# Optimization experiments

Measured on AMD Instinct MI355X. Metric: run time of the kernel, lower is better.

Reference implementation:

```python
import jax, jax.numpy as jnp
import numpy as np

N_EMBD = 1024
N_HEAD = 16


def setup_inputs() -> dict:
    key = jax.random.key(0)
    k1, k2, k3 = jax.random.split(key, 3)
    B, T, C = 4, 2048, N_EMBD
    x = jax.random.normal(k1, (B, T, C), dtype=jnp.float32)
    # params (bias=False)
    w_attn = jax.random.normal(k2, (C, 3 * C), dtype=jnp.float32) * (C ** -0.5)
    w_proj = jax.random.normal(k3, (C, C), dtype=jnp.float32) * (C ** -0.5)
    return {"x": x, "w_attn": w_attn, "w_proj": w_proj}


def reference(x, w_attn, w_proj):
    B, T, C = x.shape
    H = N_HEAD
    hs = C // H
    qkv = x @ w_attn  # [B,T,3C]
    q, k, v = jnp.split(qkv, 3, axis=-1)
    # [B,H,T,hs]
    q = q.reshape(B, T, H, hs).transpose(0, 2, 1, 3)
    k = k.reshape(B, T, H, hs).transpose(0, 2, 1, 3)
    v = v.reshape(B, T, H, hs).transpose(0, 2, 1, 3)
    wei = jnp.einsum('bhqd,bhkd->bhqk', q, k) * (hs ** -0.5)
    causal = jnp.tril(jnp.ones((T, T), dtype=bool))
    wei = jnp.where(causal[None, None], wei, -jnp.inf)
    wei = jax.nn.softmax(wei, axis=-1)
    # dropout p=0.0 -> identity
    y = jnp.einsum('bhqk,bhkd->bhqd', wei, v)
    y = y.transpose(0, 2, 1, 3).reshape(B, T, C)
    return y @ w_proj
```

## Files before the change

### kernel.cpp

```cpp
#include <hip/hip_runtime.h>
#include <math.h>
#include <stdint.h>

#define B_BATCH 4
#define T_SEQ   2048
#define C_EMB   1024
#define NH      16
#define HS      64

typedef _Float16 half_t;
typedef __attribute__((ext_vector_type(8))) _Float16 half8;
typedef __attribute__((ext_vector_type(4))) _Float16 half4;
typedef __attribute__((ext_vector_type(2))) __fp16 pk16x2;
typedef __attribute__((ext_vector_type(4))) float f32x4;

static __device__ __forceinline__ f32x4 mfma_k16(half4 a, half4 b, f32x4 c) {
#if __has_builtin(__builtin_amdgcn_mfma_f32_16x16x16f16)
    return __builtin_amdgcn_mfma_f32_16x16x16f16(a, b, c, 0, 0, 0);
#else
    half8 a8 = {a.x, a.y, a.z, a.w, (_Float16)0, (_Float16)0, (_Float16)0, (_Float16)0};
    half8 b8 = {b.x, b.y, b.z, b.w, (_Float16)0, (_Float16)0, (_Float16)0, (_Float16)0};
    return __builtin_amdgcn_mfma_f32_16x16x32_f16(a8, b8, c, 0, 0, 0);
#endif
}

static __device__ __forceinline__ void stage16(const void* g, void* lds_base) {
#if __has_builtin(__builtin_amdgcn_global_load_lds)
    __builtin_amdgcn_global_load_lds(
        (const __attribute__((address_space(1))) void*)g,
        (__attribute__((address_space(3))) void*)lds_base, 16, 0, 0);
#else
    const int lane = threadIdx.x & 63;
    ((uint4*)lds_base)[lane] = *(const uint4*)g;
#endif
}

__global__ __launch_bounds__(256) void prep_kernel(const float* __restrict__ x,
                                                   half_t* __restrict__ xh,
                                                   const float* __restrict__ wa,
                                                   half_t* __restrict__ waT,
                                                   const float* __restrict__ wp,
                                                   half_t* __restrict__ wpT) {
    const int blk = blockIdx.x;
    const int tid = threadIdx.x;

    if (blk < 4096) {
        const int i = blk * 256 + tid;
        const float4 a = *(const float4*)(x + (size_t)i * 8);
        const float4 b = *(const float4*)(x + (size_t)i * 8 + 4);
        const pk16x2 h0 = __builtin_amdgcn_cvt_pkrtz(a.x, a.y);
        const pk16x2 h1 = __builtin_amdgcn_cvt_pkrtz(a.z, a.w);
        const pk16x2 h2 = __builtin_amdgcn_cvt_pkrtz(b.x, b.y);
        const pk16x2 h3 = __builtin_amdgcn_cvt_pkrtz(b.z, b.w);
        half8 o = {(_Float16)h0.x, (_Float16)h0.y, (_Float16)h1.x, (_Float16)h1.y,
                   (_Float16)h2.x, (_Float16)h2.y, (_Float16)h3.x, (_Float16)h3.y};
        *(half8*)(xh + (size_t)i * 8) = o;
        return;
    }

    const float* W;
    half_t* WT;
    int K, N, bb;
    if (blk < 4096 + 768) {
        bb = blk - 4096; W = wa; WT = waT; K = 1024; N = 3072;
    } else {
        bb = blk - 4864; W = wp; WT = wpT; K = 1024; N = 1024;
    }
    const int ntiles = N / 64;
    const int n0 = (bb % ntiles) * 64;
    const int k0 = (bb / ntiles) * 64;

    __shared__ float t[64][65];
    const int r = tid >> 4, c4 = (tid & 15) * 4;
#pragma unroll
    for (int p = 0; p < 4; ++p) {
        const float4 g = *(const float4*)(W + (size_t)(k0 + p * 16 + r) * N + n0 + c4);
        t[p * 16 + r][c4 + 0] = g.x;
        t[p * 16 + r][c4 + 1] = g.y;
        t[p * 16 + r][c4 + 2] = g.z;
        t[p * 16 + r][c4 + 3] = g.w;
    }
    __syncthreads();
#pragma unroll
    for (int p = 0; p < 4; ++p) {
        const int n = p * 16 + r;
        half4 s = {(_Float16)t[c4 + 0][n], (_Float16)t[c4 + 1][n],
                   (_Float16)t[c4 + 2][n], (_Float16)t[c4 + 3][n]};
        *(half4*)(WT + (size_t)(n0 + n) * K + k0 + c4) = s;
    }
}

#define BK2 64

__global__ __launch_bounds__(512, 2) void gemm256(const half_t* __restrict__ A,
                                                  const half_t* __restrict__ Bt,
                                                  half_t* __restrict__ Cout,
                                                  int M, int N, int K) {
    __shared__ __align__(16) half_t SM[65536];

    const int tid  = threadIdx.x;
    const int lane = tid & 63;
    const int wid  = tid >> 6;
    const int l16  = lane & 15;
    const int quad = lane >> 4;

    const int nwg = gridDim.x;
    const int cpx = nwg >> 3;
    const int bid = (blockIdx.x & 7) * cpx + (blockIdx.x >> 3);
    const int nbx = N >> 8;
    const int bx = bid % nbx;
    const int by = bid / nbx;
    const size_t m0 = (size_t)by << 8;
    const size_t n0 = (size_t)bx << 8;

    const int warpM = (wid >> 2) * 128;
    const int wn    = (wid & 3) * 64;
    const int NTk   = K >> 6;

    const int srow = tid >> 3;
    const int scsw = (tid & 7) ^ (srow & 7);
    const half_t* gAs = A  + (m0 + srow) * (size_t)K + scsw * 8;
    const half_t* gBs = Bt + (n0 + srow) * (size_t)K + scsw * 8;

    f32x4 acc[8][4];
#pragma unroll
    for (int i = 0; i < 8; ++i)
#pragma unroll
        for (int j = 0; j < 4; ++j) acc[i][j] = (f32x4){0.f, 0.f, 0.f, 0.f};

    auto ldA = [&](const half_t* Ab, int mt, int kk) -> half8 {
        const int r = warpM + mt * 16 + l16;
        const int c = (kk * 4 + quad) ^ (l16 & 7);
        return *(const half8*)(Ab + r * 64 + c * 8);
    };
    auto ldB = [&](const half_t* Bb, int nt, int kk) -> half8 {
        const int r = wn + nt * 16 + l16;
        const int c = (kk * 4 + quad) ^ (l16 & 7);
        return *(const half8*)(Bb + r * 64 + c * 8);
    };

#pragma unroll
    for (int s = 0; s < 4; ++s)
        stage16(gAs + (size_t)(s * 64) * K, SM + s * 4096 + wid * 512);
#pragma unroll
    for (int s = 0; s < 4; ++s)
        stage16(gBs + (size_t)(s * 64) * K, SM + 16384 + s * 4096 + wid * 512);
    if (NTk > 1) {
#pragma unroll
        for (int s = 0; s < 4; ++s)
            stage16(gBs + (size_t)(s * 64) * K + BK2, SM + 49152 + s * 4096 + wid * 512);
        asm volatile("s_waitcnt vmcnt(4)" ::: "memory");
    } else {
        asm volatile("s_waitcnt vmcnt(0)" ::: "memory");
    }
    __builtin_amdgcn_s_barrier();
    __builtin_amdgcn_sched_barrier(0);

    auto tile_body = [&](int t, half_t* Ac, half_t* Bc, half_t* An) {
        const int kA = (t + 1) * BK2;
        const int kB = (t + 2) * BK2;
        const bool doA = (t + 1) < NTk;
        const bool doB = (t + 2) < NTk;

        half8 fb[4][2];

        if (doA) {
            stage16(gAs + (size_t)(0 * 64) * K + kA, An + 0 * 4096 + wid * 512);
            stage16(gAs + (size_t)(1 * 64) * K + kA, An + 1 * 4096 + wid * 512);
        }
#pragma unroll
        for (int nt = 0; nt < 4; ++nt) {
            fb[nt][0] = ldB(Bc, nt, 0);
            fb[nt][1] = ldB(Bc, nt, 1);
        }
        {
            half8 a00 = ldA(Ac, 0, 0), a01 = ldA(Ac, 0, 1);
            half8 a10 = ldA(Ac, 1, 0), a11 = ldA(Ac, 1, 1);
            __builtin_amdgcn_s_barrier();
            __builtin_amdgcn_s_setprio(1);
#pragma unroll
            for (int nt = 0; nt < 4; ++nt) {
                acc[0][nt] = __builtin_amdgcn_mfma_f32_16x16x32_f16(a00, fb[nt][0], acc[0][nt], 0, 0, 0);
                acc[0][nt] = __builtin_amdgcn_mfma_f32_16x16x32_f16(a01, fb[nt][1], acc[0][nt], 0, 0, 0);
                acc[1][nt] = __builtin_amdgcn_mfma_f32_16x16x32_f16(a10, fb[nt][0], acc[1][nt], 0, 0, 0);
                acc[1][nt] = __builtin_amdgcn_mfma_f32_16x16x32_f16(a11, fb[nt][1], acc[1][nt], 0, 0, 0);
            }
            __builtin_amdgcn_s_setprio(0);
        }
        if (doA) {
            stage16(gAs + (size_t)(2 * 64) * K + kA, An + 2 * 4096 + wid * 512);
            stage16(gAs + (size_t)(3 * 64) * K + kA, An + 3 * 4096 + wid * 512);
        }
        {
            half8 a00 = ldA(Ac, 2, 0), a01 = ldA(Ac, 2, 1);
            half8 a10 = ldA(Ac, 3, 0), a11 = ldA(Ac, 3, 1);
            __builtin_amdgcn_s_barrier();
            __builtin_amdgcn_s_setprio(1);
#pragma unroll
            for (int nt = 0; nt < 4; ++nt) {
                acc[2][nt] = __builtin_amdgcn_mfma_f32_16x16x32_f16(a00, fb[nt][0], acc[2][nt], 0, 0, 0);
                acc[2][nt] = __builtin_amdgcn_mfma_f32_16x16x32_f16(a01, fb[nt][1], acc[2][nt], 0, 0, 0);
                acc[3][nt] = __builtin_amdgcn_mfma_f32_16x16x32_f16(a10, fb[nt][0], acc[3][nt], 0, 0, 0);
                acc[3][nt] = __builtin_amdgcn_mfma_f32_16x16x32_f16(a11, fb[nt][1], acc[3][nt], 0, 0, 0);
            }
            __builtin_amdgcn_s_setprio(0);
        }
        if (doB) {
            stage16(gBs + (size_t)(0 * 64) * K + kB, Bc + 0 * 4096 + wid * 512);
            stage16(gBs + (size_t)(1 * 64) * K + kB, Bc + 1 * 4096 + wid * 512);
        }
        {
            half8 a00 = ldA(Ac, 4, 0), a01 = ldA(Ac, 4, 1);
            half8 a10 = ldA(Ac, 5, 0), a11 = ldA(Ac, 5, 1);
            __builtin_amdgcn_s_barrier();
            __builtin_amdgcn_s_setprio(1);
#pragma unroll
            for (int nt = 0; nt < 4; ++nt) {
                acc[4][nt] = __builtin_amdgcn_mfma_f32_16x16x32_f16(a00, fb[nt][0], acc[4][nt], 0, 0, 0);
                acc[4][nt] = __builtin_amdgcn_mfma_f32_16x16x32_f16(a01, fb[nt][1], acc[4][nt], 0, 0, 0);
                acc[5][nt] = __builtin_amdgcn_mfma_f32_16x16x32_f16(a10, fb[nt][0], acc[5][nt], 0, 0, 0);
                acc[5][nt] = __builtin_amdgcn_mfma_f32_16x16x32_f16(a11, fb[nt][1], acc[5][nt], 0, 0, 0);
            }
            __builtin_amdgcn_s_setprio(0);
        }
        if (doB) {
            stage16(gBs + (size_t)(2 * 64) * K + kB, Bc + 2 * 4096 + wid * 512);
            stage16(gBs + (size_t)(3 * 64) * K + kB, Bc + 3 * 4096 + wid * 512);
        }
        {
            half8 a00 = ldA(Ac, 6, 0), a01 = ldA(Ac, 6, 1);
            half8 a10 = ldA(Ac, 7, 0), a11 = ldA(Ac, 7, 1);
            __builtin_amdgcn_s_barrier();
            __builtin_amdgcn_s_setprio(1);
#pragma unroll
            for (int nt = 0; nt < 4; ++nt) {
                acc[6][nt] = __builtin_amdgcn_mfma_f32_16x16x32_f16(a00, fb[nt][0], acc[6][nt], 0, 0, 0);
                acc[6][nt] = __builtin_amdgcn_mfma_f32_16x16x32_f16(a01, fb[nt][1], acc[6][nt], 0, 0, 0);
                acc[7][nt] = __builtin_amdgcn_mfma_f32_16x16x32_f16(a10, fb[nt][0], acc[7][nt], 0, 0, 0);
                acc[7][nt] = __builtin_amdgcn_mfma_f32_16x16x32_f16(a11, fb[nt][1], acc[7][nt], 0, 0, 0);
            }
            __builtin_amdgcn_s_setprio(0);
        }
        if (doB) {
            asm volatile("s_waitcnt vmcnt(4)" ::: "memory");
        } else if (doA) {
            asm volatile("s_waitcnt vmcnt(0)" ::: "memory");
        }
        __builtin_amdgcn_s_barrier();
        __builtin_amdgcn_sched_barrier(0);
    };

    for (int tt = 0; tt < NTk; tt += 2) {
        tile_body(tt, SM, SM + 16384, SM + 32768);
        if (tt + 1 < NTk)
            tile_body(tt + 1, SM + 32768, SM + 49152, SM);
    }

    __syncthreads();
    float* cw = (float*)SM + wid * 1024;
    const int rrow = lane >> 2;
    const int cseg = (lane & 3) * 16;
#pragma unroll
    for (int mt = 0; mt < 8; ++mt) {
#pragma unroll
        for (int nt = 0; nt < 4; ++nt)
            *(f32x4*)&cw[(nt * 16 + l16) * 16 + quad * 4] = acc[mt][nt];
        half_t tmp[16];
#pragma unroll
        for (int jj = 0; jj < 16; ++jj)
            tmp[jj] = (half_t)cw[(cseg + jj) * 16 + rrow];
        half_t* dst = Cout + (m0 + warpM + mt * 16 + rrow) * (size_t)N + n0 + wn + cseg;
        *(half8*)(dst)     = *(const half8*)(tmp);
        *(half8*)(dst + 8) = *(const half8*)(tmp + 8);
    }
}

__global__ __launch_bounds__(512, 2) void gemm128f(const half_t* __restrict__ A,
                                                   const half_t* __restrict__ Bt,
                                                   float* __restrict__ Cout,
                                                   int M, int N, int K) {
    __shared__ __align__(16) half_t SM[49152];

    const int tid  = threadIdx.x;
    const int lane = tid & 63;
    const int wid  = tid >> 6;
    const int l16  = lane & 15;
    const int quad = lane >> 4;

    const int nwg = gridDim.x;
    const int cpx = nwg >> 3;
    const int bid = (blockIdx.x & 7) * cpx + (blockIdx.x >> 3);
    const int nbx = N >> 8;
    const int bx = bid % nbx;
    const int by = bid / nbx;
    const size_t m0 = (size_t)by << 7;
    const size_t n0 = (size_t)bx << 8;

    const int warpM = (wid >> 2) * 64;
    const int wn    = (wid & 3) * 64;
    const int NTk   = K >> 6;

    const int srow = tid >> 3;
    const int scsw = (tid & 7) ^ (srow & 7);
    const half_t* gAs = A  + (m0 + srow) * (size_t)K + scsw * 8;
    const half_t* gBs = Bt + (n0 + srow) * (size_t)K + scsw * 8;

    half_t* const A0 = SM;
    half_t* const B0 = SM + 8192;
    half_t* const A1 = SM + 24576;
    half_t* const B1 = SM + 32768;

    f32x4 acc[4][4];
#pragma unroll
    for (int i = 0; i < 4; ++i)
#pragma unroll
        for (int j = 0; j < 4; ++j) acc[i][j] = (f32x4){0.f, 0.f, 0.f, 0.f};

    auto ldA = [&](const half_t* Ab, int mt, int kk) -> half8 {
        const int r = warpM + mt * 16 + l16;
        const int c = (kk * 4 + quad) ^ (l16 & 7);
        return *(const half8*)(Ab + r * 64 + c * 8);
    };
    auto ldB = [&](const half_t* Bb, int nt, int kk) -> half8 {
        const int r = wn + nt * 16 + l16;
        const int c = (kk * 4 + quad) ^ (l16 & 7);
        return *(const half8*)(Bb + r * 64 + c * 8);
    };

#pragma unroll
    for (int s = 0; s < 2; ++s)
        stage16(gAs + (size_t)(s * 64) * K, A0 + s * 4096 + wid * 512);
#pragma unroll
    for (int s = 0; s < 4; ++s)
        stage16(gBs + (size_t)(s * 64) * K, B0 + s * 4096 + wid * 512);
    if (NTk > 1) {
#pragma unroll
        for (int s = 0; s < 4; ++s)
            stage16(gBs + (size_t)(s * 64) * K + BK2, B1 + s * 4096 + wid * 512);
        asm volatile("s_waitcnt vmcnt(4)" ::: "memory");
    } else {
        asm volatile("s_waitcnt vmcnt(0)" ::: "memory");
    }
    __builtin_amdgcn_s_barrier();
    __builtin_amdgcn_sched_barrier(0);

    auto tile_body = [&](int t, half_t* Ac, half_t* Bc, half_t* An) {
        const int kA = (t + 1) * BK2;
        const int kB = (t + 2) * BK2;
        const bool doA = (t + 1) < NTk;
        const bool doB = (t + 2) < NTk;

        half8 fb[4][2];

        if (doA) {
            stage16(gAs + (size_t)(0 * 64) * K + kA, An + 0 * 4096 + wid * 512);
            stage16(gAs + (size_t)(1 * 64) * K + kA, An + 1 * 4096 + wid * 512);
        }
#pragma unroll
        for (int nt = 0; nt < 4; ++nt) {
            fb[nt][0] = ldB(Bc, nt, 0);
            fb[nt][1] = ldB(Bc, nt, 1);
        }
        {
            half8 a00 = ldA(Ac, 0, 0), a01 = ldA(Ac, 0, 1);
            half8 a10 = ldA(Ac, 1, 0), a11 = ldA(Ac, 1, 1);
            __builtin_amdgcn_s_barrier();
            __builtin_amdgcn_s_setprio(1);
#pragma unroll
            for (int nt = 0; nt < 4; ++nt) {
                acc[0][nt] = __builtin_amdgcn_mfma_f32_16x16x32_f16(a00, fb[nt][0], acc[0][nt], 0, 0, 0);
                acc[0][nt] = __builtin_amdgcn_mfma_f32_16x16x32_f16(a01, fb[nt][1], acc[0][nt], 0, 0, 0);
                acc[1][nt] = __builtin_amdgcn_mfma_f32_16x16x32_f16(a10, fb[nt][0], acc[1][nt], 0, 0, 0);
                acc[1][nt] = __builtin_amdgcn_mfma_f32_16x16x32_f16(a11, fb[nt][1], acc[1][nt], 0, 0, 0);
            }
            __builtin_amdgcn_s_setprio(0);
        }
        if (doB) {
#pragma unroll
            for (int s = 0; s < 4; ++s)
                stage16(gBs + (size_t)(s * 64) * K + kB, Bc + s * 4096 + wid * 512);
        }
        {
            half8 a00 = ldA(Ac, 2, 0), a01 = ldA(Ac, 2, 1);
            half8 a10 = ldA(Ac, 3, 0), a11 = ldA(Ac, 3, 1);
            __builtin_amdgcn_s_barrier();
            __builtin_amdgcn_s_setprio(1);
#pragma unroll
            for (int nt = 0; nt < 4; ++nt) {
                acc[2][nt] = __builtin_amdgcn_mfma_f32_16x16x32_f16(a00, fb[nt][0], acc[2][nt], 0, 0, 0);
                acc[2][nt] = __builtin_amdgcn_mfma_f32_16x16x32_f16(a01, fb[nt][1], acc[2][nt], 0, 0, 0);
                acc[3][nt] = __builtin_amdgcn_mfma_f32_16x16x32_f16(a10, fb[nt][0], acc[3][nt], 0, 0, 0);
                acc[3][nt] = __builtin_amdgcn_mfma_f32_16x16x32_f16(a11, fb[nt][1], acc[3][nt], 0, 0, 0);
            }
            __builtin_amdgcn_s_setprio(0);
        }
        if (doB) {
            asm volatile("s_waitcnt vmcnt(4)" ::: "memory");
        } else if (doA) {
            asm volatile("s_waitcnt vmcnt(0)" ::: "memory");
        }
        __builtin_amdgcn_s_barrier();
        __builtin_amdgcn_sched_barrier(0);
    };

    for (int tt = 0; tt < NTk; tt += 2) {
        tile_body(tt, A0, B0, A1);
        if (tt + 1 < NTk)
            tile_body(tt + 1, A1, B1, A0);
    }

#pragma unroll
    for (int mt = 0; mt < 4; ++mt)
#pragma unroll
        for (int nt = 0; nt < 4; ++nt)
#pragma unroll
            for (int r = 0; r < 4; ++r) {
                const size_t row = m0 + warpM + mt * 16 + quad * 4 + r;
                const size_t col = n0 + wn + nt * 16 + l16;
                Cout[row * (size_t)N + col] = acc[mt][nt][r];
            }
}

#define SCALE_EXP2 0.18033688f

__global__ __launch_bounds__(256, 4) void attn_mfma(const half_t* __restrict__ qkv,
                                                    half_t* __restrict__ y) {
    __shared__ __align__(16) half_t Kl[64 * 64];
    __shared__ __align__(16) half_t Vt[64 * 64];
    __shared__ float Lstat[64];

    const int tid  = threadIdx.x;
    const int wid  = tid >> 6;
    const int lane = tid & 63;
    const int l16  = lane & 15;
    const int quad = lane >> 4;

    const int L = blockIdx.x;
    const int g = L & 63;
    const int s = L >> 6;
    const int h = g & 15;
    const int b = g >> 4;

    const size_t rs = 3 * C_EMB;
    const half_t* qb = qkv + (size_t)b * T_SEQ * rs + h * HS;
    const half_t* kb = qb + C_EMB;
    const half_t* vb = qb + 2 * C_EMB;

    const int srow = tid >> 2;
    const int scol = (tid & 3) * 16;
    const int sc2  = (tid & 3) * 2;
    const int rp   = tid & 31;
    const int dblk = tid >> 5;

    const int qrel = wid * 16 + l16;

    auto kswz = [&](int row, int chunk) -> half_t* {
        return Kl + row * 64 + ((chunk ^ (row & 7)) << 3);
    };
    auto vswz = [&](int row, int chunk) -> half_t* {
        return Vt + row * 64 + ((chunk ^ (row & 7)) << 3);
    };

#pragma unroll 1
    for (int j = 0; j < 2; ++j) {
        const int qh = (j == 0) ? (31 - s) : s;
        const int q0 = qh * 64;

        __syncthreads();
        {
            const half_t* src = qb + (size_t)(q0 + srow) * rs + scol;
            const half8 q0r = *(const half8*)(src);
            const half8 q1r = *(const half8*)(src + 8);
            *(half8*)kswz(srow, sc2)     = q0r;
            *(half8*)kswz(srow, sc2 + 1) = q1r;
        }
        half8 kp0, kp1;
        uint4 vpa, vpc;
        {
            const half_t* ksrc = kb + (size_t)srow * rs + scol;
            kp0 = *(const half8*)(ksrc);
            kp1 = *(const half8*)(ksrc + 8);
            const half_t* vsrc = vb + (size_t)(2 * rp) * rs + dblk * 8;
            vpa = *(const uint4*)(vsrc);
            vpc = *(const uint4*)(vsrc + rs);
        }
        __syncthreads();

        half8 aQ[2];
        aQ[0] = *(const half8*)kswz(wid * 16 + l16, quad);
        aQ[1] = *(const half8*)kswz(wid * 16 + l16, 4 + quad);

        f32x4 O[4];
#pragma unroll
        for (int dt = 0; dt < 4; ++dt) O[dt] = (f32x4){0.f, 0.f, 0.f, 0.f};
        float lw = 0.f;

        for (int kt = 0; kt <= qh; ++kt) {
            const bool diag = (kt == qh);
            __syncthreads();

            *(half8*)kswz(srow, sc2)     = kp0;
            *(half8*)kswz(srow, sc2 + 1) = kp1;
            {
                const uint32_t a0[4] = {vpa.x, vpa.y, vpa.z, vpa.w};
                const uint32_t c0[4] = {vpc.x, vpc.y, vpc.z, vpc.w};
#pragma unroll
                for (int u = 0; u < 4; ++u) {
                    const int d0 = dblk * 8 + 2 * u;
                    const uint32_t w0 = (a0[u] & 0xffffu) | (c0[u] << 16);
                    const uint32_t w1 = (a0[u] >> 16) | (c0[u] & 0xffff0000u);
                    *(uint32_t*)((unsigned short*)vswz(d0,     rp >> 2) + (rp & 3) * 2) = w0;
                    *(uint32_t*)((unsigned short*)vswz(d0 + 1, rp >> 2) + (rp & 3) * 2) = w1;
                }
            }
            __syncthreads();

            if (kt < qh) {
                const int kn = (kt + 1) * 64;
                const half_t* ksrc = kb + (size_t)(kn + srow) * rs + scol;
                kp0 = *(const half8*)(ksrc);
                kp1 = *(const half8*)(ksrc + 8);
                const half_t* vsrc = vb + (size_t)(kn + 2 * rp) * rs + dblk * 8;
                vpa = *(const uint4*)(vsrc);
                vpc = *(const uint4*)(vsrc + rs);
            }

#pragma unroll
            for (int mt = 0; mt < 4; ++mt) {
                const half8 aK0 = *(const half8*)kswz(mt * 16 + l16, quad);
                const half8 aK1 = *(const half8*)kswz(mt * 16 + l16, 4 + quad);
                f32x4 sa = (f32x4){0.f, 0.f, 0.f, 0.f};
                sa = __builtin_amdgcn_mfma_f32_16x16x32_f16(aK0, aQ[0], sa, 0, 0, 0);
                sa = __builtin_amdgcn_mfma_f32_16x16x32_f16(aK1, aQ[1], sa, 0, 0, 0);

                const int kbase = mt * 16 + quad * 4;
                float p[4];
#pragma unroll
                for (int r = 0; r < 4; ++r)
                    p[r] = __builtin_amdgcn_exp2f(sa[r] * SCALE_EXP2);
                if (diag) {
#pragma unroll
                    for (int r = 0; r < 4; ++r)
                        if (kbase + r > qrel) p[r] = 0.f;
                }
                lw += (p[0] + p[1]) + (p[2] + p[3]);

                const half4 pa = {(_Float16)p[0], (_Float16)p[1],
                                  (_Float16)p[2], (_Float16)p[3]};
#pragma unroll
                for (int dt = 0; dt < 4; ++dt) {
                    const half_t* pv = vswz(dt * 16 + l16, 2 * mt + (quad >> 1)) +
                                       (quad & 1) * 4;
                    const half4 bV = *(const half4*)pv;
                    O[dt] = mfma_k16(pa, bV, O[dt]);
                }
            }
        }

        lw += __shfl_xor(lw, 16);
        lw += __shfl_xor(lw, 32);
        if (quad == 0) Lstat[wid * 16 + l16] = lw;
        __syncthreads();
#pragma unroll
        for (int r = 0; r < 4; ++r) {
            const int rowl = wid * 16 + quad * 4 + r;
            const float inv = 1.f / Lstat[rowl];
#pragma unroll
            for (int dt = 0; dt < 4; ++dt)
                *(vswz(rowl, 2 * dt + (l16 >> 3)) + (l16 & 7)) =
                    (half_t)(O[dt][r] * inv);
        }
        __syncthreads();
        {
            half_t* dst = y + ((size_t)b * T_SEQ + q0 + srow) * C_EMB + h * HS + scol;
            *(half8*)(dst)     = *(const half8*)vswz(srow, sc2);
            *(half8*)(dst + 8) = *(const half8*)vswz(srow, sc2 + 1);
        }
    }
}

extern "C" void kernel_launch(void* const* d_in, const int* in_sizes, int n_in,
                              void* d_out, int out_size, void* d_ws, size_t ws_size,
                              hipStream_t stream) {
    const float* x      = (const float*)d_in[0];
    const float* w_attn = (const float*)d_in[1];
    const float* w_proj = (const float*)d_in[2];
    float* out = (float*)d_out;

    half_t* xh   = (half_t*)d_ws;
    half_t* waT  = xh   + (size_t)8192 * 1024;
    half_t* wpT  = waT  + (size_t)3072 * 1024;
    half_t* qkvh = wpT  + (size_t)1024 * 1024;
    half_t* yh   = qkvh + (size_t)8192 * 3072;

    prep_kernel<<<5120, 256, 0, stream>>>(x, xh, w_attn, waT, w_proj, wpT);

    gemm256<<<dim3(384), 512, 0, stream>>>(xh, waT, qkvh, 8192, 3072, 1024);

    attn_mfma<<<dim3(1024), 256, 0, stream>>>(qkvh, yh);

    gemm128f<<<dim3(256), 512, 0, stream>>>(yh, wpT, out, 8192, 1024, 1024);
}
```

Baseline: 253.7 us.

## Enlarge attention query tile to 128 rows per block for K/V reuse

```diff
diff --git a/kernel.cpp b/kernel.cpp
--- a/kernel.cpp
+++ b/kernel.cpp
@@ -423,11 +423,11 @@
 
 #define SCALE_EXP2 0.18033688f
 
-__global__ __launch_bounds__(256, 4) void attn_mfma(const half_t* __restrict__ qkv,
+__global__ __launch_bounds__(256, 2) void attn_mfma(const half_t* __restrict__ qkv,
                                                     half_t* __restrict__ y) {
     __shared__ __align__(16) half_t Kl[64 * 64];
     __shared__ __align__(16) half_t Vt[64 * 64];
-    __shared__ float Lstat[64];
+    __shared__ float Lstat[128];
 
     const int tid  = threadIdx.x;
     const int wid  = tid >> 6;
@@ -452,7 +452,7 @@
     const int rp   = tid & 31;
     const int dblk = tid >> 5;
 
-    const int qrel = wid * 16 + l16;
+    const int wq = wid * 32;
 
     auto kswz = [&](int row, int chunk) -> half_t* {
         return Kl + row * 64 + ((chunk ^ (row & 7)) << 3);
@@ -463,40 +463,35 @@
 
 #pragma unroll 1
     for (int j = 0; j < 2; ++j) {
-        const int qh = (j == 0) ? (31 - s) : s;
-        const int q0 = qh * 64;
-
-        __syncthreads();
-        {
-            const half_t* src = qb + (size_t)(q0 + srow) * rs + scol;
-            const half8 q0r = *(const half8*)(src);
-            const half8 q1r = *(const half8*)(src + 8);
-            *(half8*)kswz(srow, sc2)     = q0r;
-            *(half8*)kswz(srow, sc2 + 1) = q1r;
-        }
+        const int jj = (j == 0) ? (15 - s) : s;
+        const int q0 = jj * 128;
+        const int ntk = 2 * jj + 2;
+
+        half8 aQ[2][2];
+#pragma unroll
+        for (int qs = 0; qs < 2; ++qs)
+#pragma unroll
+            for (int s2 = 0; s2 < 2; ++s2)
+                aQ[qs][s2] = *(const half8*)(qb +
+                    (size_t)(q0 + wq + qs * 16 + l16) * rs + s2 * 32 + quad * 8);
+
+        const half_t* kptr = kb + (size_t)srow * rs + scol;
+        const half_t* vptr = vb + (size_t)(2 * rp) * rs + dblk * 8;
         half8 kp0, kp1;
         uint4 vpa, vpc;
-        {
-            const half_t* ksrc = kb + (size_t)srow * rs + scol;
-            kp0 = *(const half8*)(ksrc);
-            kp1 = *(const half8*)(ksrc + 8);
-            const half_t* vsrc = vb + (size_t)(2 * rp) * rs + dblk * 8;
-            vpa = *(const uint4*)(vsrc);
-            vpc = *(const uint4*)(vsrc + rs);
-        }
-        __syncthreads();
-
-        half8 aQ[2];
-        aQ[0] = *(const half8*)kswz(wid * 16 + l16, quad);
-        aQ[1] = *(const half8*)kswz(wid * 16 + l16, 4 + quad);
-
-        f32x4 O[4];
-#pragma unroll
-        for (int dt = 0; dt < 4; ++dt) O[dt] = (f32x4){0.f, 0.f, 0.f, 0.f};
-        float lw = 0.f;
-
-        for (int kt = 0; kt <= qh; ++kt) {
-            const bool diag = (kt == qh);
+        kp0 = *(const half8*)(kptr);
+        kp1 = *(const half8*)(kptr + 8);
+        vpa = *(const uint4*)(vptr);
+        vpc = *(const uint4*)(vptr + rs);
+
+        f32x4 O[2][4];
+#pragma unroll
+        for (int qs = 0; qs < 2; ++qs)
+#pragma unroll
+            for (int dt = 0; dt < 4; ++dt) O[qs][dt] = (f32x4){0.f, 0.f, 0.f, 0.f};
+        float lw[2] = {0.f, 0.f};
+
+        for (int kt = 0; kt < ntk; ++kt) {
             __syncthreads();
 
             *(half8*)kswz(srow, sc2)     = kp0;
@@ -515,64 +510,99 @@
             }
             __syncthreads();
 
-            if (kt < qh) {
-                const int kn = (kt + 1) * 64;
-                const half_t* ksrc = kb + (size_t)(kn + srow) * rs + scol;
-                kp0 = *(const half8*)(ksrc);
-                kp1 = *(const half8*)(ksrc + 8);
-                const half_t* vsrc = vb + (size_t)(kn + 2 * rp) * rs + dblk * 8;
-                vpa = *(const uint4*)(vsrc);
-                vpc = *(const uint4*)(vsrc + rs);
-            }
+            if (kt + 1 < ntk) {
+                kptr += 64 * rs;
+                vptr += 64 * rs;
+                kp0 = *(const half8*)(kptr);
+                kp1 = *(const half8*)(kptr + 8);
+                vpa = *(const uint4*)(vptr);
+                vpc = *(const uint4*)(vptr + rs);
+            }
+
+            const bool dmask = (kt >= ntk - 2);
 
 #pragma unroll
             for (int mt = 0; mt < 4; ++mt) {
                 const half8 aK0 = *(const half8*)kswz(mt * 16 + l16, quad);
                 const half8 aK1 = *(const half8*)kswz(mt * 16 + l16, 4 + quad);
-                f32x4 sa = (f32x4){0.f, 0.f, 0.f, 0.f};
-                sa = __builtin_amdgcn_mfma_f32_16x16x32_f16(aK0, aQ[0], sa, 0, 0, 0);
-                sa = __builtin_amdgcn_mfma_f32_16x16x32_f16(aK1, aQ[1], sa, 0, 0, 0);
-
-                const int kbase = mt * 16 + quad * 4;
-                float p[4];
-#pragma unroll
-                for (int r = 0; r < 4; ++r)
-                    p[r] = __builtin_amdgcn_exp2f(sa[r] * SCALE_EXP2);
-                if (diag) {
+                half4 bV[4];
+#pragma unroll
+                for (int dt = 0; dt < 4; ++dt)
+                    bV[dt] = *(const half4*)(vswz(dt * 16 + l16, 2 * mt + (quad >> 1)) +
+                                             (quad & 1) * 4);
+                const int kbase = kt * 64 + mt * 16 + quad * 4;
+#pragma unroll
+                for (int qs = 0; qs < 2; ++qs) {
+                    f32x4 sa = (f32x4){0.f, 0.f, 0.f, 0.f};
+                    sa = __builtin_amdgcn_mfma_f32_16x16x32_f16(aK0, aQ[qs][0], sa, 0, 0, 0);
+                    sa = __builtin_amdgcn_mfma_f32_16x16x32_f16(aK1, aQ[qs][1], sa, 0, 0, 0);
+
+                    float p[4];
 #pragma unroll
                     for (int r = 0; r < 4; ++r)
-                        if (kbase + r > qrel) p[r] = 0.f;
+                        p[r] = __builtin_amdgcn_exp2f(sa[r] * SCALE_EXP2);
+                    if (dmask) {
+                        const int qg = q0 + wq + qs * 16 + l16;
+#pragma unroll
+                        for (int r = 0; r < 4; ++r)
+                            if (kbase + r > qg) p[r] = 0.f;
+                    }
+                    lw[qs] += (p[0] + p[1]) + (p[2] + p[3]);
+
+                    const half4 pa = {(_Float16)p[0], (_Float16)p[1],
+                                      (_Float16)p[2], (_Float16)p[3]};
+#pragma unroll
+                    for (int dt = 0; dt < 4; ++dt)
+                        O[qs][dt] = mfma_k16(pa, bV[dt], O[qs][dt]);
                 }
-                lw += (p[0] + p[1]) + (p[2] + p[3]);
-
-                const half4 pa = {(_Float16)p[0], (_Float16)p[1],
-                                  (_Float16)p[2], (_Float16)p[3]};
-#pragma unroll
-                for (int dt = 0; dt < 4; ++dt) {
-                    const half_t* pv = vswz(dt * 16 + l16, 2 * mt + (quad >> 1)) +
-                                       (quad & 1) * 4;
-                    const half4 bV = *(const half4*)pv;
-                    O[dt] = mfma_k16(pa, bV, O[dt]);
+            }
+        }
+
+#pragma unroll
+        for (int qs = 0; qs < 2; ++qs) {
+            lw[qs] += __shfl_xor(lw[qs], 16);
+            lw[qs] += __shfl_xor(lw[qs], 32);
+            if (quad == 0) Lstat[wq + qs * 16 + l16] = lw[qs];
+        }
+        __syncthreads();
+
+        if (wid < 2) {
+#pragma unroll
+            for (int qs = 0; qs < 2; ++qs)
+#pragma unroll
+                for (int r = 0; r < 4; ++r) {
+                    const int rowl = wq + qs * 16 + quad * 4 + r;
+                    const float inv = 1.f / Lstat[rowl];
+#pragma unroll
+                    for (int dt = 0; dt < 4; ++dt)
+                        *(vswz(rowl, 2 * dt + (l16 >> 3)) + (l16 & 7)) =
+                            (half_t)(O[qs][dt][r] * inv);
                 }
-            }
-        }
-
-        lw += __shfl_xor(lw, 16);
-        lw += __shfl_xor(lw, 32);
-        if (quad == 0) Lstat[wid * 16 + l16] = lw;
+        }
         __syncthreads();
-#pragma unroll
-        for (int r = 0; r < 4; ++r) {
-            const int rowl = wid * 16 + quad * 4 + r;
-            const float inv = 1.f / Lstat[rowl];
-#pragma unroll
-            for (int dt = 0; dt < 4; ++dt)
-                *(vswz(rowl, 2 * dt + (l16 >> 3)) + (l16 & 7)) =
-                    (half_t)(O[dt][r] * inv);
+        {
+            half_t* dst = y + ((size_t)b * T_SEQ + q0 + srow) * C_EMB + h * HS + scol;
+            *(half8*)(dst)     = *(const half8*)vswz(srow, sc2);
+            *(half8*)(dst + 8) = *(const half8*)vswz(srow, sc2 + 1);
         }
         __syncthreads();
-        {
-            half_t* dst = y + ((size_t)b * T_SEQ + q0 + srow) * C_EMB + h * HS + scol;
+
+        if (wid >= 2) {
+#pragma unroll
+            for (int qs = 0; qs < 2; ++qs)
+#pragma unroll
+                for (int r = 0; r < 4; ++r) {
+                    const int rowg = wq + qs * 16 + quad * 4 + r;
+                    const float inv = 1.f / Lstat[rowg];
+#pragma unroll
+                    for (int dt = 0; dt < 4; ++dt)
+                        *(vswz(rowg - 64, 2 * dt + (l16 >> 3)) + (l16 & 7)) =
+                            (half_t)(O[qs][dt][r] * inv);
+                }
+        }
+        __syncthreads();
+        {
+            half_t* dst = y + ((size_t)b * T_SEQ + q0 + 64 + srow) * C_EMB + h * HS + scol;
             *(half8*)(dst)     = *(const half8*)vswz(srow, sc2);
             *(half8*)(dst + 8) = *(const half8*)vswz(srow, sc2 + 1);
         }
@@ -597,7 +627,7 @@
 
     gemm256<<<dim3(384), 512, 0, stream>>>(xh, waT, qkvh, 8192, 3072, 1024);
 
-    attn_mfma<<<dim3(1024), 256, 0, stream>>>(qkvh, yh);
+    attn_mfma<<<dim3(512), 256, 0, stream>>>(qkvh, yh);
 
     gemm128f<<<dim3(256), 512, 0, stream>>>(yh, wpT, out, 8192, 1024, 1024);
 }
```

Measured after the change: 249.1 us. About the same (-1.8%).
